# Performance work log

Hardware: AMD Instinct MI355X
Metric: run time of the kernel (lower is better)

The kernel has to match this reference:

```python
import jax, jax.numpy as jnp
import numpy as np
import math

V, T, E, H, L = 32000, 1024, 1024, 16, 6
B = 2
D = E // H
F = 4 * E


def setup_inputs() -> dict:
    key = jax.random.key(0)
    ks = jax.random.split(key, 12)
    s = 0.02
    rn = lambda k, shape: jax.random.normal(k, shape, jnp.float32) * s
    return dict(
        idx=jax.random.randint(ks[0], (B, T), 0, V),
        tok_w=rn(ks[1], (V, E)),
        pos_w=rn(ks[2], (T, E)),
        ln1_g=jnp.ones((L, E)), ln1_b=jnp.zeros((L, E)),
        wq=rn(ks[3], (L, E, E)), wk=rn(ks[4], (L, E, E)), wv=rn(ks[5], (L, E, E)),
        wp=rn(ks[6], (L, E, E)), bp=jnp.zeros((L, E)),
        ln2_g=jnp.ones((L, E)), ln2_b=jnp.zeros((L, E)),
        w1=rn(ks[7], (L, E, F)), b1=jnp.zeros((L, F)),
        w2=rn(ks[8], (L, F, E)), b2=jnp.zeros((L, E)),
        lnf_g=jnp.ones((E,)), lnf_b=jnp.zeros((E,)),
        wlm=rn(ks[9], (E, V)), blm=jnp.zeros((V,)),
    )


def _layernorm(x, g, b, eps=1e-5):
    m = jnp.mean(x, axis=-1, keepdims=True)
    v = jnp.var(x, axis=-1, keepdims=True)
    return (x - m) * jax.lax.rsqrt(v + eps) * g + b


def _forward(idx, tok_w, pos_w, ln1_g, ln1_b, wq, wk, wv, wp, bp,
             ln2_g, ln2_b, w1, b1, w2, b2, lnf_g, lnf_b, wlm, blm):
    Bx, Tx = idx.shape
    x = tok_w[idx] + pos_w[jnp.arange(Tx)][None, :, :]  # [B,T,E]
    causal = jnp.tril(jnp.ones((Tx, Tx), dtype=bool))
    scale = 1.0 / math.sqrt(D)
    for l in range(L):
        h = _layernorm(x, ln1_g[l], ln1_b[l])
        q = (h @ wq[l]).reshape(Bx, Tx, H, D).transpose(0, 2, 1, 3)  # [B,H,T,D]
        k = (h @ wk[l]).reshape(Bx, Tx, H, D).transpose(0, 2, 1, 3)
        v = (h @ wv[l]).reshape(Bx, Tx, H, D).transpose(0, 2, 1, 3)
        att = jnp.einsum('bhtd,bhsd->bhts', q, k) * scale  # [B,H,T,T]
        att = jnp.where(causal, att, -jnp.inf)
        att = jax.nn.softmax(att, axis=-1)
        y = jnp.einsum('bhts,bhsd->bhtd', att, v)
        y = y.transpose(0, 2, 1, 3).reshape(Bx, Tx, E)
        x = x + y @ wp[l] + bp[l]
        h2 = _layernorm(x, ln2_g[l], ln2_b[l])
        ff = jax.nn.gelu(h2 @ w1[l] + b1[l], approximate=False) @ w2[l] + b2[l]
        x = x + ff
    x = _layernorm(x, lnf_g, lnf_b)
    return x @ wlm + blm  # logits [B,T,V]


def reference(idx, tok_w, pos_w, ln1_g, ln1_b, wq, wk, wv, wp, bp,
              ln2_g, ln2_b, w1, b1, w2, b2, lnf_g, lnf_b, wlm, blm):
    return _forward(idx, tok_w, pos_w, ln1_g, ln1_b, wq, wk, wv, wp, bp,
                    ln2_g, ln2_b, w1, b1, w2, b2, lnf_g, lnf_b, wlm, blm)
```

## Files before the change

kernel.cpp:

```cpp
#include <hip/hip_runtime.h>

#define T_SEQ   1024
#define E_DIM   1024
#define H_HEADS 16
#define D_HEAD  64
#define L_LAYERS 6
#define B_BATCH 2
#define F_DIM   4096
#define V_VOCAB 32000

typedef float f32x4 __attribute__((ext_vector_type(4)));
typedef short short8 __attribute__((ext_vector_type(8)));

__device__ __forceinline__ unsigned short f2bf(float f) {
  union { float f; unsigned int u; } v; v.f = f;
  unsigned int r = v.u + 0x7fffu + ((v.u >> 16) & 1u);
  return (unsigned short)(r >> 16);
}

#define GLDS16(gp, lp) __builtin_amdgcn_global_load_lds( \
    (const __attribute__((address_space(1))) void*)(gp), \
    (__attribute__((address_space(3))) void*)(lp), 16, 0, 0)

__global__ void embed_kernel(const int* __restrict__ idx, const float* __restrict__ tok,
                             const float* __restrict__ pos, float* __restrict__ x) {
  int i = blockIdx.x * 256 + threadIdx.x;
  int bt = i >> 8;
  int e4 = i & 255;
  int t  = bt & (T_SEQ - 1);
  int tokid = idx[bt];
  f32x4 a = *(const f32x4*)(tok + (size_t)tokid * E_DIM + e4 * 4);
  f32x4 p = *(const f32x4*)(pos + (size_t)t * E_DIM + e4 * 4);
  *(f32x4*)(x + (size_t)bt * E_DIM + e4 * 4) = a + p;
}

__global__ void ln_kernel(const float* __restrict__ x, const float* __restrict__ g,
                          const float* __restrict__ b, unsigned short* __restrict__ out) {
  int row = blockIdx.x;
  int tid = threadIdx.x;
  const float* xr = x + (size_t)row * E_DIM;
  f32x4 v = *(const f32x4*)(xr + tid * 4);
  float s  = v[0] + v[1] + v[2] + v[3];
  float s2 = v[0]*v[0] + v[1]*v[1] + v[2]*v[2] + v[3]*v[3];
  #pragma unroll
  for (int off = 32; off > 0; off >>= 1) {
    s  += __shfl_xor(s,  off);
    s2 += __shfl_xor(s2, off);
  }
  __shared__ float red[2][4];
  int wave = tid >> 6;
  if ((tid & 63) == 0) { red[0][wave] = s; red[1][wave] = s2; }
  __syncthreads();
  s  = red[0][0] + red[0][1] + red[0][2] + red[0][3];
  s2 = red[1][0] + red[1][1] + red[1][2] + red[1][3];
  float mean = s * (1.0f / E_DIM);
  float var  = s2 * (1.0f / E_DIM) - mean * mean;
  float rstd = rsqrtf(var + 1e-5f);
  f32x4 gv = *(const f32x4*)(g + tid * 4);
  f32x4 bv = *(const f32x4*)(b + tid * 4);
  ushort4 o;
  o.x = f2bf((v[0] - mean) * rstd * gv[0] + bv[0]);
  o.y = f2bf((v[1] - mean) * rstd * gv[1] + bv[1]);
  o.z = f2bf((v[2] - mean) * rstd * gv[2] + bv[2]);
  o.w = f2bf((v[3] - mean) * rstd * gv[3] + bv[3]);
  *(ushort4*)(out + (size_t)row * E_DIM + tid * 4) = o;
}

__device__ __forceinline__ void wtrans_body(const float* __restrict__ W,
    unsigned short* __restrict__ Wt, int K, int N, int bx, int by) {
  __shared__ float tile[64][65];
  const int n0 = bx * 64, k0 = by * 64;
  const int tr  = threadIdx.x >> 4;
  const int tc4 = (threadIdx.x & 15) * 4;
  #pragma unroll
  for (int p = 0; p < 4; ++p) {
    f32x4 v = *(const f32x4*)(W + (size_t)(k0 + p * 16 + tr) * N + n0 + tc4);
    tile[p * 16 + tr][tc4 + 0] = v[0];
    tile[p * 16 + tr][tc4 + 1] = v[1];
    tile[p * 16 + tr][tc4 + 2] = v[2];
    tile[p * 16 + tr][tc4 + 3] = v[3];
  }
  __syncthreads();
  #pragma unroll
  for (int p = 0; p < 4; ++p) {
    int n = p * 16 + tr;
    ushort4 o;
    o.x = f2bf(tile[tc4 + 0][n]);
    o.y = f2bf(tile[tc4 + 1][n]);
    o.z = f2bf(tile[tc4 + 2][n]);
    o.w = f2bf(tile[tc4 + 3][n]);
    *(ushort4*)(Wt + (size_t)(n0 + n) * K + k0 + tc4) = o;
  }
}

__global__ __launch_bounds__(256) void wtrans_kernel(const float* __restrict__ W,
    unsigned short* __restrict__ Wt, int K, int N) {
  wtrans_body(W, Wt, K, N, blockIdx.x, blockIdx.y);
}

__global__ __launch_bounds__(256) void wtrans4_kernel(const float* __restrict__ W0,
    const float* __restrict__ W1, const float* __restrict__ W2, const float* __restrict__ W3,
    unsigned short* __restrict__ Wt) {
  const float* W = blockIdx.z == 0 ? W0 : (blockIdx.z == 1 ? W1 : (blockIdx.z == 2 ? W2 : W3));
  wtrans_body(W, Wt + (size_t)blockIdx.z * E_DIM * E_DIM, E_DIM, E_DIM,
              blockIdx.x, blockIdx.y);
}

__global__ __launch_bounds__(256) void wtrans2_kernel(const float* __restrict__ W1,
    const float* __restrict__ W2, unsigned short* __restrict__ Wt1,
    unsigned short* __restrict__ Wt2) {
  const int id = blockIdx.x;
  if (blockIdx.y == 0) wtrans_body(W1, Wt1, E_DIM, F_DIM, id % (F_DIM / 64), id / (F_DIM / 64));
  else                 wtrans_body(W2, Wt2, F_DIM, E_DIM, id % (E_DIM / 64), id / (E_DIM / 64));
}

__global__ __launch_bounds__(256) void attn_mfma_kernel(
    const unsigned short* __restrict__ qkv, unsigned short* __restrict__ y) {
  __shared__ __align__(16) unsigned short Kl[64 * 64];
  __shared__ __align__(16) unsigned short Vt[64 * 64];
  __shared__ __align__(16) unsigned short pbuf[4][16][72];
  const int tid  = threadIdx.x;
  const int lane = tid & 63;
  const int wave = tid >> 6;
  const int h  = blockIdx.y & (H_HEADS - 1);
  const int b  = blockIdx.y >> 4;
  const int r0 = blockIdx.x * 64 + wave * 16;
  const size_t RS = 3 * E_DIM;
  const unsigned short* q = qkv + (size_t)b * T_SEQ * RS + (size_t)h * D_HEAD;
  const unsigned short* k = q + E_DIM;
  const unsigned short* v = q + 2 * E_DIM;
  const size_t ybase = (size_t)b * T_SEQ * E_DIM + (size_t)h * D_HEAD;
  const int fr = lane & 15, fg = lane >> 4;
  const int rsw = (fr & 7) << 4;

  const int krow = lane >> 3;
  const int kcol = ((lane & 7) * 16) ^ ((krow & 7) << 4);

  short8 aq[2];
  #pragma unroll
  for (int c = 0; c < 2; ++c)
    aq[c] = *(const short8*)(q + (size_t)(r0 + fr) * RS + c * 32 + fg * 8);

  f32x4 oacc[4];
  #pragma unroll
  for (int cg = 0; cg < 4; ++cg) oacc[cg] = (f32x4){0.f, 0.f, 0.f, 0.f};
  float m_ = -1e30f, l_ = 0.0f;

  char* pb = (char*)pbuf + wave * 16 * 144;
  const int ntiles = blockIdx.x + 1;
  for (int t = 0; t < ntiles; ++t) {
    const int j0 = t * 64;
    __syncthreads();
    #pragma unroll
    for (int i = 0; i < 2; ++i) {
      const int row = wave * 16 + i * 8;
      GLDS16((const char*)k + (size_t)(j0 + row + krow) * RS * 2 + kcol,
             (char*)Kl + row * 128);
    }
    {
      short8 v0 = *(const short8*)(v + (size_t)(j0 + lane) * RS + wave * 16);
      short8 v1 = *(const short8*)(v + (size_t)(j0 + lane) * RS + wave * 16 + 8);
      #pragma unroll
      for (int i = 0; i < 8; ++i) {
        const int d0 = wave * 16 + i;
        *(unsigned short*)((char*)Vt + ((d0 * 128 + lane * 2) ^ ((d0 & 7) << 4))) =
            (unsigned short)v0[i];
        const int d1 = wave * 16 + 8 + i;
        *(unsigned short*)((char*)Vt + ((d1 * 128 + lane * 2) ^ ((d1 & 7) << 4))) =
            (unsigned short)v1[i];
      }
    }
    __syncthreads();
    f32x4 st[4];
    #pragma unroll
    for (int c = 0; c < 4; ++c) {
      const char* kb = (char*)Kl + (c * 16 + fr) * 128;
      short8 ka0 = *(const short8*)(kb + ((fg * 16) ^ rsw));
      short8 ka1 = *(const short8*)(kb + ((64 + fg * 16) ^ rsw));
      f32x4 z = (f32x4){0.f, 0.f, 0.f, 0.f};
      z = __builtin_amdgcn_mfma_f32_16x16x32_bf16(ka0, aq[0], z, 0, 0, 0);
      z = __builtin_amdgcn_mfma_f32_16x16x32_bf16(ka1, aq[1], z, 0, 0, 0);
      st[c] = z;
    }
    const int qg = r0 + fr;
    float pv[4][4];
    float mx = -1e30f;
    #pragma unroll
    for (int c = 0; c < 4; ++c)
      #pragma unroll
      for (int r = 0; r < 4; ++r) {
        const int kj = j0 + c * 16 + fg * 4 + r;
        float val = (kj <= qg) ? st[c][r] * 0.125f : -1e30f;
        pv[c][r] = val;
        mx = fmaxf(mx, val);
      }
    mx = fmaxf(mx, __shfl_xor(mx, 16));
    mx = fmaxf(mx, __shfl_xor(mx, 32));
    const float mn = fmaxf(m_, mx);
    const float cfs = __expf(m_ - mn);
    float ls = 0.0f;
    #pragma unroll
    for (int c = 0; c < 4; ++c) {
      ushort4 o;
      float e0 = __expf(pv[c][0] - mn), e1 = __expf(pv[c][1] - mn);
      float e2 = __expf(pv[c][2] - mn), e3 = __expf(pv[c][3] - mn);
      ls += (e0 + e1) + (e2 + e3);
      o.x = f2bf(e0); o.y = f2bf(e1); o.z = f2bf(e2); o.w = f2bf(e3);
      *(ushort4*)(pb + fr * 144 + c * 32 + fg * 8) = o;
    }
    ls += __shfl_xor(ls, 16);
    ls += __shfl_xor(ls, 32);
    l_ = l_ * cfs + ls;
    m_ = mn;
    float cfO[4];
    #pragma unroll
    for (int r = 0; r < 4; ++r) cfO[r] = __shfl(cfs, (lane & 48) | (fg * 4 + r));
    asm volatile("s_waitcnt lgkmcnt(0)" ::: "memory");
    __builtin_amdgcn_sched_barrier(0);
    short8 pa0 = *(const short8*)(pb + fr * 144 + fg * 16);
    short8 pa1 = *(const short8*)(pb + fr * 144 + 64 + fg * 16);
    __builtin_amdgcn_s_setprio(1);
    #pragma unroll
    for (int cg = 0; cg < 4; ++cg) {
      const char* vb = (char*)Vt + (cg * 16 + fr) * 128;
      short8 b0 = *(const short8*)(vb + ((fg * 16) ^ rsw));
      short8 b1 = *(const short8*)(vb + ((64 + fg * 16) ^ rsw));
      #pragma unroll
      for (int r = 0; r < 4; ++r) oacc[cg][r] *= cfO[r];
      oacc[cg] = __builtin_amdgcn_mfma_f32_16x16x32_bf16(pa0, b0, oacc[cg], 0, 0, 0);
      oacc[cg] = __builtin_amdgcn_mfma_f32_16x16x32_bf16(pa1, b1, oacc[cg], 0, 0, 0);
    }
    __builtin_amdgcn_s_setprio(0);
  }
  float lO[4];
  #pragma unroll
  for (int r = 0; r < 4; ++r) lO[r] = __shfl(l_, (lane & 48) | (fg * 4 + r));
  #pragma unroll
  for (int cg = 0; cg < 4; ++cg)
    #pragma unroll
    for (int r = 0; r < 4; ++r)
      y[ybase + (size_t)(r0 + fg * 4 + r) * E_DIM + cg * 16 + fr] = f2bf(oacc[cg][r] / lO[r]);
}

template<int BM, int BN, bool HAS_BIAS, bool GELU_ACT, bool HAS_RES, bool OUT_BF16>
__global__ __launch_bounds__(256) void gemm_bt_kernel(
    const unsigned short* __restrict__ A, const unsigned short* __restrict__ Bt,
    const float* __restrict__ bias, const float* __restrict__ res,
    void* __restrict__ out, int M, int N, int K) {
  constexpr int BK = 64;
  constexpr int MR = BM / 32;
  constexpr int NR = BN / 32;
  constexpr int AI = BM / 32;
  constexpr int BI = BN / 32;
  __shared__ __align__(16) unsigned short As[BM * BK];
  __shared__ __align__(16) unsigned short Bs[BN * BK];
  const int tid  = threadIdx.x;
  const int lane = tid & 63;
  const int wave = tid >> 6;
  const int wr = wave >> 1, wc = wave & 1;

  const int mt = M / BM;
  const int q8 = gridDim.x >> 3;
  const int g  = (blockIdx.x & 7) * q8 + (blockIdx.x >> 3);
  const int m0 = (g % mt) * BM, n0 = (g / mt) * BN;

  const int fr = lane & 15, fg = lane >> 4;
  const int lrow = lane >> 3;
  const int scol = ((lane & 7) * 16) ^ (lrow << 4);
  const size_t K2 = (size_t)K * 2;
  const char* aG = (const char*)A  + (size_t)(m0 + wave * 8 + lrow) * K2 + scol;
  const char* bG = (const char*)Bt + (size_t)(n0 + wave * 8 + lrow) * K2 + scol;

  f32x4 acc[MR][NR];
  #pragma unroll
  for (int mi = 0; mi < MR; ++mi)
    #pragma unroll
    for (int ni = 0; ni < NR; ++ni) acc[mi][ni] = (f32x4){0.f, 0.f, 0.f, 0.f};

  for (int k0 = 0; k0 < K; k0 += BK) {
    __syncthreads();
    #pragma unroll
    for (int i = 0; i < AI; ++i)
      GLDS16(aG + (size_t)i * 32 * K2 + (size_t)k0 * 2, (char*)As + wave * 1024 + i * 4096);
    #pragma unroll
    for (int i = 0; i < BI; ++i)
      GLDS16(bG + (size_t)i * 32 * K2 + (size_t)k0 * 2, (char*)Bs + wave * 1024 + i * 4096);
    __syncthreads();

    short8 af[MR][2], bf[NR][2];
    #pragma unroll
    for (int mi = 0; mi < MR; ++mi) {
      const int row = wr * (BM / 2) + mi * 16 + fr;
      #pragma unroll
      for (int kh = 0; kh < 2; ++kh)
        af[mi][kh] = *(const short8*)((const char*)As + row * 128 +
                       ((kh * 64 + fg * 16) ^ ((row & 7) << 4)));
    }
    #pragma unroll
    for (int ni = 0; ni < NR; ++ni) {
      const int row = wc * (BN / 2) + ni * 16 + fr;
      #pragma unroll
      for (int kh = 0; kh < 2; ++kh)
        bf[ni][kh] = *(const short8*)((const char*)Bs + row * 128 +
                       ((kh * 64 + fg * 16) ^ ((row & 7) << 4)));
    }
    #pragma unroll
    for (int mi = 0; mi < MR; ++mi)
      #pragma unroll
      for (int ni = 0; ni < NR; ++ni) {
        acc[mi][ni] = __builtin_amdgcn_mfma_f32_16x16x32_bf16(af[mi][0], bf[ni][0], acc[mi][ni], 0, 0, 0);
        acc[mi][ni] = __builtin_amdgcn_mfma_f32_16x16x32_bf16(af[mi][1], bf[ni][1], acc[mi][ni], 0, 0, 0);
      }
  }

  #pragma unroll
  for (int mi = 0; mi < MR; ++mi) {
    #pragma unroll
    for (int ni = 0; ni < NR; ++ni) {
      const int col = n0 + wc * (BN / 2) + ni * 16 + fr;
      float bv = HAS_BIAS ? bias[col] : 0.0f;
      #pragma unroll
      for (int r = 0; r < 4; ++r) {
        const int row = m0 + wr * (BM / 2) + mi * 16 + fg * 4 + r;
        float val = acc[mi][ni][r] + bv;
        if (GELU_ACT) val = 0.5f * val * (1.0f + erff(val * 0.70710678118f));
        if (HAS_RES)  val += res[(size_t)row * N + col];
        if (OUT_BF16) ((unsigned short*)out)[(size_t)row * N + col] = f2bf(val);
        else          ((float*)out)[(size_t)row * N + col] = val;
      }
    }
  }
}

__global__ __launch_bounds__(512, 1) void gemm8p_kernel(
    const unsigned short* __restrict__ A, const unsigned short* __restrict__ Bt,
    const float* __restrict__ bias, float* __restrict__ out, int M, int N, int K) {
  __shared__ __align__(16) char lds[131072];
  const int tid  = threadIdx.x;
  const int lane = tid & 63;
  const int wv   = tid >> 6;
  const int wm = wv >> 2, wn = wv & 3;

  const int mt = M >> 8;
  const int q8 = gridDim.x >> 3;
  const int g  = (blockIdx.x & 7) * q8 + (blockIdx.x >> 3);
  const int m0 = (g % mt) * 256, n0 = (g / mt) * 256;

  const int fr = lane & 15, fg = lane >> 4;
  const size_t K2 = (size_t)K * 2;
  const int nIter = K >> 7;

  const int csw0 = (fg * 16) ^ ((fr & 7) << 4);
  const int csw1 = (64 + fg * 16) ^ ((fr & 7) << 4);

  const int sc = (lane * 16) & 127;
  const size_t laneoff = (size_t)(lane >> 3) * K2 + (size_t)(sc ^ ((lane >> 3) << 4));
  const char* Asrc = (const char*)(A + (size_t)m0 * K) + (size_t)(wv * 8) * K2 + laneoff;
  const char* Bsrc = (const char*)(Bt + (size_t)n0 * K) + laneoff;

  f32x4 acc[8][4];
  #pragma unroll
  for (int i = 0; i < 8; ++i)
    #pragma unroll
    for (int j = 0; j < 4; ++j) acc[i][j] = (f32x4){0.f, 0.f, 0.f, 0.f};

  auto stageA = [&](int b, int q, int kt) {
    GLDS16(Asrc + (size_t)(q * 64) * K2 + (size_t)kt * 128,
           lds + b * 65536 + q * 8192 + wv * 1024);
  };
  auto stageB = [&](int b, int j, int o, int kt) {
    const int gw = j * 64 + wv * 8;
    const int rw = ((gw >> 5) << 6) + (gw & 31) + o * 32;
    GLDS16(Bsrc + (size_t)rw * K2 + (size_t)kt * 128,
           lds + b * 65536 + 32768 + rw * 128);
  };

  stageA(0, 0, 0); stageA(0, 2, 0);
  stageB(0, 0, 0, 0); stageB(0, 1, 0, 0);
  stageA(0, 1, 0); stageA(0, 3, 0);
  stageB(0, 0, 1, 0); stageB(0, 1, 1, 0);
  stageA(1, 0, 1); stageA(1, 2, 1);
  stageB(1, 0, 0, 1); stageB(1, 1, 0, 1);
  __builtin_amdgcn_sched_barrier(0);
  asm volatile("s_waitcnt vmcnt(4)" ::: "memory");
  __builtin_amdgcn_s_barrier();

  for (int i = 0; i < nIter; ++i) {
    const bool last = (i == nIter - 1);
    short8 fa[4][2];
    #pragma unroll
    for (int p = 0; p < 8; ++p) {
      const int b  = p >> 2;
      const int mh = (p & 3) >> 1;
      const int nh = p & 1;
      const char* Ab = lds + b * 65536;
      const char* Bb = Ab + 32768;
      __builtin_amdgcn_sched_barrier(0);
      if (nh == 0) {
        #pragma unroll
        for (int j = 0; j < 4; ++j) {
          const int row = wm * 128 + mh * 64 + j * 16 + fr;
          fa[j][0] = *(const short8*)(Ab + row * 128 + csw0);
          fa[j][1] = *(const short8*)(Ab + row * 128 + csw1);
        }
      }
      short8 fb[2][2];
      #pragma unroll
      for (int n = 0; n < 2; ++n) {
        const int row = wn * 64 + nh * 32 + n * 16 + fr;
        fb[n][0] = *(const short8*)(Bb + row * 128 + csw0);
        fb[n][1] = *(const short8*)(Bb + row * 128 + csw1);
      }
      if (p == 0) { stageA(1, 1, 2 * i + 1); stageA(1, 3, 2 * i + 1); }
      if (p == 1) { stageB(1, 0, 1, 2 * i + 1); stageB(1, 1, 1, 2 * i + 1); }
      if (!last) {
        if (p == 2) { stageA(0, 0, 2 * i + 2); stageA(0, 2, 2 * i + 2); }
        if (p == 3) { stageB(0, 0, 0, 2 * i + 2); stageB(0, 1, 0, 2 * i + 2); }
        if (p == 4) { stageA(0, 1, 2 * i + 2); stageA(0, 3, 2 * i + 2); }
        if (p == 5) { stageB(0, 0, 1, 2 * i + 2); stageB(0, 1, 1, 2 * i + 2); }
        if (p == 6) { stageA(1, 0, 2 * i + 3); stageA(1, 2, 2 * i + 3); }
        if (p == 7) { stageB(1, 0, 0, 2 * i + 3); stageB(1, 1, 0, 2 * i + 3); }
      }
      __builtin_amdgcn_sched_barrier(0);
      __builtin_amdgcn_s_barrier();
      __builtin_amdgcn_sched_barrier(0);
      __builtin_amdgcn_s_setprio(1);
      #pragma unroll
      for (int j = 0; j < 4; ++j)
        #pragma unroll
        for (int n = 0; n < 2; ++n) {
          acc[mh * 4 + j][nh * 2 + n] = __builtin_amdgcn_mfma_f32_16x16x32_bf16(
              fa[j][0], fb[n][0], acc[mh * 4 + j][nh * 2 + n], 0, 0, 0);
          acc[mh * 4 + j][nh * 2 + n] = __builtin_amdgcn_mfma_f32_16x16x32_bf16(
              fa[j][1], fb[n][1], acc[mh * 4 + j][nh * 2 + n], 0, 0, 0);
        }
      __builtin_amdgcn_s_setprio(0);
      __builtin_amdgcn_sched_barrier(0);
      if (p == 3) {
        if (!last) asm volatile("s_waitcnt vmcnt(4)" ::: "memory");
        else       asm volatile("s_waitcnt vmcnt(0)" ::: "memory");
      }
      if (p == 7 && !last)
        asm volatile("s_waitcnt vmcnt(4)" ::: "memory");
      __builtin_amdgcn_s_barrier();
    }
  }

  #pragma unroll
  for (int mi = 0; mi < 8; ++mi) {
    #pragma unroll
    for (int ni = 0; ni < 4; ++ni) {
      const int col = n0 + wn * 64 + ni * 16 + fr;
      const float bv = bias[col];
      #pragma unroll
      for (int r = 0; r < 4; ++r) {
        const int row = m0 + wm * 128 + mi * 16 + fg * 4 + r;
        out[(size_t)row * N + col] = acc[mi][ni][r] + bv;
      }
    }
  }
}

extern "C" void kernel_launch(void* const* d_in, const int* in_sizes, int n_in,
                              void* d_out, int out_size, void* d_ws, size_t ws_size,
                              hipStream_t stream) {
  const int*   idx   = (const int*)  d_in[0];
  const float* tok_w = (const float*)d_in[1];
  const float* pos_w = (const float*)d_in[2];
  const float* ln1_g = (const float*)d_in[3];
  const float* ln1_b = (const float*)d_in[4];
  const float* wq    = (const float*)d_in[5];
  const float* wk    = (const float*)d_in[6];
  const float* wv    = (const float*)d_in[7];
  const float* wp    = (const float*)d_in[8];
  const float* bp    = (const float*)d_in[9];
  const float* ln2_g = (const float*)d_in[10];
  const float* ln2_b = (const float*)d_in[11];
  const float* w1    = (const float*)d_in[12];
  const float* b1    = (const float*)d_in[13];
  const float* w2    = (const float*)d_in[14];
  const float* b2    = (const float*)d_in[15];
  const float* lnf_g = (const float*)d_in[16];
  const float* lnf_b = (const float*)d_in[17];
  const float* wlm   = (const float*)d_in[18];
  const float* blm   = (const float*)d_in[19];

  const int M = B_BATCH * T_SEQ;
  const size_t EE = (size_t)E_DIM * E_DIM;
  const size_t EF = (size_t)E_DIM * F_DIM;
  char* p = (char*)d_ws;
  float* x            = (float*)p;          p += (size_t)M * E_DIM * 4;
  unsigned short* hb  = (unsigned short*)p; p += (size_t)M * E_DIM * 2;
  unsigned short* qkv = (unsigned short*)p; p += (size_t)M * 3 * E_DIM * 2;
  unsigned short* yb  = (unsigned short*)p; p += (size_t)M * E_DIM * 2;
  unsigned short* tb  = (unsigned short*)p; p += (size_t)M * F_DIM * 2;
  unsigned short* wtb = (unsigned short*)p; p += (size_t)V_VOCAB * E_DIM * 2;

  embed_kernel<<<M * E_DIM / 4 / 256, 256, 0, stream>>>(idx, tok_w, pos_w, x);

  dim3 g_a(T_SEQ / 64, B_BATCH * H_HEADS);
  for (int l = 0; l < L_LAYERS; ++l) {
    ln_kernel<<<M, 256, 0, stream>>>(x, ln1_g + (size_t)l * E_DIM, ln1_b + (size_t)l * E_DIM, hb);
    wtrans4_kernel<<<dim3(E_DIM / 64, E_DIM / 64, 4), 256, 0, stream>>>(
        wq + l * EE, wk + l * EE, wv + l * EE, wp + l * EE, wtb);
    gemm_bt_kernel<128, 128, false, false, false, true>
        <<<(M / 128) * (3 * E_DIM / 128), 256, 0, stream>>>(
        hb, wtb, nullptr, nullptr, qkv, M, 3 * E_DIM, E_DIM);
    attn_mfma_kernel<<<g_a, 256, 0, stream>>>(qkv, yb);
    gemm_bt_kernel<64, 128, true, false, true, false>
        <<<(M / 64) * (E_DIM / 128), 256, 0, stream>>>(
        yb, wtb + 3 * EE, bp + (size_t)l * E_DIM, x, x, M, E_DIM, E_DIM);
    ln_kernel<<<M, 256, 0, stream>>>(x, ln2_g + (size_t)l * E_DIM, ln2_b + (size_t)l * E_DIM, hb);
    wtrans2_kernel<<<dim3(1024, 2), 256, 0, stream>>>(
        w1 + l * EF, w2 + l * EF, wtb, wtb + EF);
    gemm_bt_kernel<128, 128, true, true, false, true>
        <<<(M / 128) * (F_DIM / 128), 256, 0, stream>>>(
        hb, wtb, b1 + (size_t)l * F_DIM, nullptr, tb, M, F_DIM, E_DIM);
    gemm_bt_kernel<64, 128, true, false, true, false>
        <<<(M / 64) * (E_DIM / 128), 256, 0, stream>>>(
        tb, wtb + EF, b2 + (size_t)l * E_DIM, x, x, M, E_DIM, F_DIM);
  }
  ln_kernel<<<M, 256, 0, stream>>>(x, lnf_g, lnf_b, hb);
  wtrans_kernel<<<dim3(V_VOCAB / 64, E_DIM / 64), 256, 0, stream>>>(wlm, wtb, E_DIM, V_VOCAB);
  gemm8p_kernel<<<(M / 256) * (V_VOCAB / 256), 512, 0, stream>>>(
      hb, wtb, blm, (float*)d_out, M, V_VOCAB, E_DIM);
}
```

Baseline: 1.404 ms.

## Write V transposed from QKV GEMM and pair causal query tiles per attention block

The QKV GEMM epilogue now writes Q and K into a 2E-stride buffer and V directly in a per-head transposed [D,T] layout. The attention kernel can then load V tiles into LDS with async global-to-LDS copies instead of doing scalar transposes. Attention blocks now hold 8 waves, pairing query tile bx with tile 15-bx so every block does the same causal work, and the grid is halved. The lm-head GEMM also reloads A fragments on every phase instead of caching them across phases, which trades register pressure against LDS traffic. Risks are uncoalesced strided V stores in the GEMM epilogue and idle waves in the paired blocks on early tiles.

```diff
diff --git a/kernel.cpp b/kernel.cpp
--- a/kernel.cpp
+++ b/kernel.cpp
@@ -114,27 +114,31 @@
   else                 wtrans_body(W2, Wt2, F_DIM, E_DIM, id % (E_DIM / 64), id / (E_DIM / 64));
 }
 
-__global__ __launch_bounds__(256) void attn_mfma_kernel(
-    const unsigned short* __restrict__ qkv, unsigned short* __restrict__ y) {
+__global__ __launch_bounds__(512) void attn_mfma_kernel(
+    const unsigned short* __restrict__ qk, const unsigned short* __restrict__ vt,
+    unsigned short* __restrict__ y) {
   __shared__ __align__(16) unsigned short Kl[64 * 64];
-  __shared__ __align__(16) unsigned short Vt[64 * 64];
-  __shared__ __align__(16) unsigned short pbuf[4][16][72];
+  __shared__ __align__(16) unsigned short Vl[64 * 64];
+  __shared__ __align__(16) unsigned short pbuf[8][16][72];
   const int tid  = threadIdx.x;
   const int lane = tid & 63;
   const int wave = tid >> 6;
+  const int grp  = wave >> 2;
+  const int wl   = wave & 3;
+  const int bx = blockIdx.x;
   const int h  = blockIdx.y & (H_HEADS - 1);
   const int b  = blockIdx.y >> 4;
-  const int r0 = blockIdx.x * 64 + wave * 16;
-  const size_t RS = 3 * E_DIM;
-  const unsigned short* q = qkv + (size_t)b * T_SEQ * RS + (size_t)h * D_HEAD;
+  const int qt = grp == 0 ? (15 - bx) : bx;
+  const int r0 = qt * 64 + wl * 16;
+  const size_t RS = 2 * E_DIM;
+  const unsigned short* q = qk + (size_t)b * T_SEQ * RS + (size_t)h * D_HEAD;
   const unsigned short* k = q + E_DIM;
-  const unsigned short* v = q + 2 * E_DIM;
+  const unsigned short* vb = vt + (size_t)(b * H_HEADS + h) * D_HEAD * T_SEQ;
   const size_t ybase = (size_t)b * T_SEQ * E_DIM + (size_t)h * D_HEAD;
   const int fr = lane & 15, fg = lane >> 4;
   const int rsw = (fr & 7) << 4;
-
-  const int krow = lane >> 3;
-  const int kcol = ((lane & 7) * 16) ^ ((krow & 7) << 4);
+  const int srow = lane >> 3;
+  const int ssw  = ((lane & 7) * 16) ^ (srow << 4);
 
   short8 aq[2];
   #pragma unroll
@@ -147,90 +151,77 @@
   float m_ = -1e30f, l_ = 0.0f;
 
   char* pb = (char*)pbuf + wave * 16 * 144;
-  const int ntiles = blockIdx.x + 1;
+  const int ntiles = 16 - bx;
   for (int t = 0; t < ntiles; ++t) {
     const int j0 = t * 64;
     __syncthreads();
-    #pragma unroll
-    for (int i = 0; i < 2; ++i) {
-      const int row = wave * 16 + i * 8;
-      GLDS16((const char*)k + (size_t)(j0 + row + krow) * RS * 2 + kcol,
-             (char*)Kl + row * 128);
+    GLDS16((const char*)k + (size_t)(j0 + wave * 8 + srow) * RS * 2 + ssw,
+           (char*)Kl + wave * 8 * 128);
+    GLDS16((const char*)vb + ((size_t)(wave * 8 + srow) * T_SEQ + j0) * 2 + ssw,
+           (char*)Vl + wave * 8 * 128);
+    __syncthreads();
+    if (t <= qt) {
+      f32x4 st[4];
+      #pragma unroll
+      for (int c = 0; c < 4; ++c) {
+        const char* kb = (char*)Kl + (c * 16 + fr) * 128;
+        short8 ka0 = *(const short8*)(kb + ((fg * 16) ^ rsw));
+        short8 ka1 = *(const short8*)(kb + ((64 + fg * 16) ^ rsw));
+        f32x4 z = (f32x4){0.f, 0.f, 0.f, 0.f};
+        z = __builtin_amdgcn_mfma_f32_16x16x32_bf16(ka0, aq[0], z, 0, 0, 0);
+        z = __builtin_amdgcn_mfma_f32_16x16x32_bf16(ka1, aq[1], z, 0, 0, 0);
+        st[c] = z;
+      }
+      const int qg = r0 + fr;
+      float pv[4][4];
+      float mx = -1e30f;
+      #pragma unroll
+      for (int c = 0; c < 4; ++c)
+        #pragma unroll
+        for (int r = 0; r < 4; ++r) {
+          const int kj = j0 + c * 16 + fg * 4 + r;
+          float val = (kj <= qg) ? st[c][r] * 0.125f : -1e30f;
+          pv[c][r] = val;
+          mx = fmaxf(mx, val);
+        }
+      mx = fmaxf(mx, __shfl_xor(mx, 16));
+      mx = fmaxf(mx, __shfl_xor(mx, 32));
+      const float mn = fmaxf(m_, mx);
+      const float cfs = __expf(m_ - mn);
+      float ls = 0.0f;
+      #pragma unroll
+      for (int c = 0; c < 4; ++c) {
+        ushort4 o;
+        float e0 = __expf(pv[c][0] - mn), e1 = __expf(pv[c][1] - mn);
+        float e2 = __expf(pv[c][2] - mn), e3 = __expf(pv[c][3] - mn);
+        ls += (e0 + e1) + (e2 + e3);
+        o.x = f2bf(e0); o.y = f2bf(e1); o.z = f2bf(e2); o.w = f2bf(e3);
+        *(ushort4*)(pb + fr * 144 + c * 32 + fg * 8) = o;
+      }
+      ls += __shfl_xor(ls, 16);
+      ls += __shfl_xor(ls, 32);
+      l_ = l_ * cfs + ls;
+      m_ = mn;
+      float cfO[4];
+      #pragma unroll
+      for (int r = 0; r < 4; ++r) cfO[r] = __shfl(cfs, (lane & 48) | (fg * 4 + r));
+      asm volatile("s_waitcnt lgkmcnt(0)" ::: "memory");
+      __builtin_amdgcn_sched_barrier(0);
+      short8 pa0 = *(const short8*)(pb + fr * 144 + fg * 16);
+      short8 pa1 = *(const short8*)(pb + fr * 144 + 64 + fg * 16);
+      __builtin_amdgcn_s_setprio(1);
+      #pragma unroll
+      for (int cg = 0; cg < 4; ++cg) {
+        const char* vv = (char*)Vl + (cg * 16 + fr) * 128;
+        short8 b0 = *(const short8*)(vv + ((fg * 16) ^ rsw));
+        short8 b1 = *(const short8*)(vv + ((64 + fg * 16) ^ rsw));
+        #pragma unroll
+        for (int r = 0; r < 4; ++r) oacc[cg][r] *= cfO[r];
+        oacc[cg] = __builtin_amdgcn_mfma_f32_16x16x32_bf16(pa0, b0, oacc[cg], 0, 0, 0);
+        oacc[cg] = __builtin_amdgcn_mfma_f32_16x16x32_bf16(pa1, b1, oacc[cg], 0, 0, 0);
+      }
+      __builtin_amdgcn_s_setprio(0);
     }
-    {
-      short8 v0 = *(const short8*)(v + (size_t)(j0 + lane) * RS + wave * 16);
-      short8 v1 = *(const short8*)(v + (size_t)(j0 + lane) * RS + wave * 16 + 8);
-      #pragma unroll
-      for (int i = 0; i < 8; ++i) {
-        const int d0 = wave * 16 + i;
-        *(unsigned short*)((char*)Vt + ((d0 * 128 + lane * 2) ^ ((d0 & 7) << 4))) =
-            (unsigned short)v0[i];
-        const int d1 = wave * 16 + 8 + i;
-        *(unsigned short*)((char*)Vt + ((d1 * 128 + lane * 2) ^ ((d1 & 7) << 4))) =
-            (unsigned short)v1[i];
-      }
-    }
-    __syncthreads();
-    f32x4 st[4];
-    #pragma unroll
-    for (int c = 0; c < 4; ++c) {
-      const char* kb = (char*)Kl + (c * 16 + fr) * 128;
-      short8 ka0 = *(const short8*)(kb + ((fg * 16) ^ rsw));
-      short8 ka1 = *(const short8*)(kb + ((64 + fg * 16) ^ rsw));
-      f32x4 z = (f32x4){0.f, 0.f, 0.f, 0.f};
-      z = __builtin_amdgcn_mfma_f32_16x16x32_bf16(ka0, aq[0], z, 0, 0, 0);
-      z = __builtin_amdgcn_mfma_f32_16x16x32_bf16(ka1, aq[1], z, 0, 0, 0);
-      st[c] = z;
-    }
-    const int qg = r0 + fr;
-    float pv[4][4];
-    float mx = -1e30f;
-    #pragma unroll
-    for (int c = 0; c < 4; ++c)
-      #pragma unroll
-      for (int r = 0; r < 4; ++r) {
-        const int kj = j0 + c * 16 + fg * 4 + r;
-        float val = (kj <= qg) ? st[c][r] * 0.125f : -1e30f;
-        pv[c][r] = val;
-        mx = fmaxf(mx, val);
-      }
-    mx = fmaxf(mx, __shfl_xor(mx, 16));
-    mx = fmaxf(mx, __shfl_xor(mx, 32));
-    const float mn = fmaxf(m_, mx);
-    const float cfs = __expf(m_ - mn);
-    float ls = 0.0f;
-    #pragma unroll
-    for (int c = 0; c < 4; ++c) {
-      ushort4 o;
-      float e0 = __expf(pv[c][0] - mn), e1 = __expf(pv[c][1] - mn);
-      float e2 = __expf(pv[c][2] - mn), e3 = __expf(pv[c][3] - mn);
-      ls += (e0 + e1) + (e2 + e3);
-      o.x = f2bf(e0); o.y = f2bf(e1); o.z = f2bf(e2); o.w = f2bf(e3);
-      *(ushort4*)(pb + fr * 144 + c * 32 + fg * 8) = o;
-    }
-    ls += __shfl_xor(ls, 16);
-    ls += __shfl_xor(ls, 32);
-    l_ = l_ * cfs + ls;
-    m_ = mn;
-    float cfO[4];
-    #pragma unroll
-    for (int r = 0; r < 4; ++r) cfO[r] = __shfl(cfs, (lane & 48) | (fg * 4 + r));
-    asm volatile("s_waitcnt lgkmcnt(0)" ::: "memory");
-    __builtin_amdgcn_sched_barrier(0);
-    short8 pa0 = *(const short8*)(pb + fr * 144 + fg * 16);
-    short8 pa1 = *(const short8*)(pb + fr * 144 + 64 + fg * 16);
-    __builtin_amdgcn_s_setprio(1);
-    #pragma unroll
-    for (int cg = 0; cg < 4; ++cg) {
-      const char* vb = (char*)Vt + (cg * 16 + fr) * 128;
-      short8 b0 = *(const short8*)(vb + ((fg * 16) ^ rsw));
-      short8 b1 = *(const short8*)(vb + ((64 + fg * 16) ^ rsw));
-      #pragma unroll
-      for (int r = 0; r < 4; ++r) oacc[cg][r] *= cfO[r];
-      oacc[cg] = __builtin_amdgcn_mfma_f32_16x16x32_bf16(pa0, b0, oacc[cg], 0, 0, 0);
-      oacc[cg] = __builtin_amdgcn_mfma_f32_16x16x32_bf16(pa1, b1, oacc[cg], 0, 0, 0);
-    }
-    __builtin_amdgcn_s_setprio(0);
   }
   float lO[4];
   #pragma unroll
@@ -242,11 +233,11 @@
       y[ybase + (size_t)(r0 + fg * 4 + r) * E_DIM + cg * 16 + fr] = f2bf(oacc[cg][r] / lO[r]);
 }
 
-template<int BM, int BN, bool HAS_BIAS, bool GELU_ACT, bool HAS_RES, bool OUT_BF16>
+template<int BM, int BN, bool HAS_BIAS, bool GELU_ACT, bool HAS_RES, int OMODE>
 __global__ __launch_bounds__(256) void gemm_bt_kernel(
     const unsigned short* __restrict__ A, const unsigned short* __restrict__ Bt,
     const float* __restrict__ bias, const float* __restrict__ res,
-    void* __restrict__ out, int M, int N, int K) {
+    void* __restrict__ out, unsigned short* __restrict__ vt, int M, int N, int K) {
   constexpr int BK = 64;
   constexpr int MR = BM / 32;
   constexpr int NR = BN / 32;
@@ -319,14 +310,37 @@
     for (int ni = 0; ni < NR; ++ni) {
       const int col = n0 + wc * (BN / 2) + ni * 16 + fr;
       float bv = HAS_BIAS ? bias[col] : 0.0f;
+      float vals[4];
+      const int rbase = m0 + wr * (BM / 2) + mi * 16 + fg * 4;
       #pragma unroll
       for (int r = 0; r < 4; ++r) {
-        const int row = m0 + wr * (BM / 2) + mi * 16 + fg * 4 + r;
         float val = acc[mi][ni][r] + bv;
         if (GELU_ACT) val = 0.5f * val * (1.0f + erff(val * 0.70710678118f));
-        if (HAS_RES)  val += res[(size_t)row * N + col];
-        if (OUT_BF16) ((unsigned short*)out)[(size_t)row * N + col] = f2bf(val);
-        else          ((float*)out)[(size_t)row * N + col] = val;
+        if (HAS_RES)  val += res[(size_t)(rbase + r) * N + col];
+        vals[r] = val;
+      }
+      if (OMODE == 0) {
+        #pragma unroll
+        for (int r = 0; r < 4; ++r)
+          ((float*)out)[(size_t)(rbase + r) * N + col] = vals[r];
+      } else if (OMODE == 1) {
+        #pragma unroll
+        for (int r = 0; r < 4; ++r)
+          ((unsigned short*)out)[(size_t)(rbase + r) * N + col] = f2bf(vals[r]);
+      } else {
+        if (col < 2 * E_DIM) {
+          #pragma unroll
+          for (int r = 0; r < 4; ++r)
+            ((unsigned short*)out)[(size_t)(rbase + r) * 2 * E_DIM + col] = f2bf(vals[r]);
+        } else {
+          const int c2 = col - 2 * E_DIM;
+          const int hh = c2 >> 6, d = c2 & 63;
+          const int bb = rbase >> 10, t0 = rbase & (T_SEQ - 1);
+          ushort4 o;
+          o.x = f2bf(vals[0]); o.y = f2bf(vals[1]);
+          o.z = f2bf(vals[2]); o.w = f2bf(vals[3]);
+          *(ushort4*)(vt + ((size_t)(bb * H_HEADS + hh) * D_HEAD + d) * T_SEQ + t0) = o;
+        }
       }
     }
   }
@@ -387,7 +401,6 @@
 
   for (int i = 0; i < nIter; ++i) {
     const bool last = (i == nIter - 1);
-    short8 fa[4][2];
     #pragma unroll
     for (int p = 0; p < 8; ++p) {
       const int b  = p >> 2;
@@ -396,15 +409,13 @@
       const char* Ab = lds + b * 65536;
       const char* Bb = Ab + 32768;
       __builtin_amdgcn_sched_barrier(0);
-      if (nh == 0) {
-        #pragma unroll
-        for (int j = 0; j < 4; ++j) {
-          const int row = wm * 128 + mh * 64 + j * 16 + fr;
-          fa[j][0] = *(const short8*)(Ab + row * 128 + csw0);
-          fa[j][1] = *(const short8*)(Ab + row * 128 + csw1);
-        }
-      }
-      short8 fb[2][2];
+      short8 fa[4][2], fb[2][2];
+      #pragma unroll
+      for (int j = 0; j < 4; ++j) {
+        const int row = wm * 128 + mh * 64 + j * 16 + fr;
+        fa[j][0] = *(const short8*)(Ab + row * 128 + csw0);
+        fa[j][1] = *(const short8*)(Ab + row * 128 + csw1);
+      }
       #pragma unroll
       for (int n = 0; n < 2; ++n) {
         const int row = wn * 64 + nh * 32 + n * 16 + fr;
@@ -491,34 +502,34 @@
   char* p = (char*)d_ws;
   float* x            = (float*)p;          p += (size_t)M * E_DIM * 4;
   unsigned short* hb  = (unsigned short*)p; p += (size_t)M * E_DIM * 2;
-  unsigned short* qkv = (unsigned short*)p; p += (size_t)M * 3 * E_DIM * 2;
+  unsigned short* qkb = (unsigned short*)p; p += (size_t)M * 2 * E_DIM * 2;
+  unsigned short* vtb = (unsigned short*)p; p += (size_t)M * E_DIM * 2;
   unsigned short* yb  = (unsigned short*)p; p += (size_t)M * E_DIM * 2;
   unsigned short* tb  = (unsigned short*)p; p += (size_t)M * F_DIM * 2;
   unsigned short* wtb = (unsigned short*)p; p += (size_t)V_VOCAB * E_DIM * 2;
 
   embed_kernel<<<M * E_DIM / 4 / 256, 256, 0, stream>>>(idx, tok_w, pos_w, x);
 
-  dim3 g_a(T_SEQ / 64, B_BATCH * H_HEADS);
   for (int l = 0; l < L_LAYERS; ++l) {
     ln_kernel<<<M, 256, 0, stream>>>(x, ln1_g + (size_t)l * E_DIM, ln1_b + (size_t)l * E_DIM, hb);
     wtrans4_kernel<<<dim3(E_DIM / 64, E_DIM / 64, 4), 256, 0, stream>>>(
         wq + l * EE, wk + l * EE, wv + l * EE, wp + l * EE, wtb);
-    gemm_bt_kernel<128, 128, false, false, false, true>
+    gemm_bt_kernel<128, 128, false, false, false, 2>
         <<<(M / 128) * (3 * E_DIM / 128), 256, 0, stream>>>(
-        hb, wtb, nullptr, nullptr, qkv, M, 3 * E_DIM, E_DIM);
-    attn_mfma_kernel<<<g_a, 256, 0, stream>>>(qkv, yb);
-    gemm_bt_kernel<64, 128, true, false, true, false>
+        hb, wtb, nullptr, nullptr, qkb, vtb, M, 3 * E_DIM, E_DIM);
+    attn_mfma_kernel<<<dim3(8, B_BATCH * H_HEADS), 512, 0, stream>>>(qkb, vtb, yb);
+    gemm_bt_kernel<64, 128, true, false, true, 0>
         <<<(M / 64) * (E_DIM / 128), 256, 0, stream>>>(
-        yb, wtb + 3 * EE, bp + (size_t)l * E_DIM, x, x, M, E_DIM, E_DIM);
+        yb, wtb + 3 * EE, bp + (size_t)l * E_DIM, x, x, nullptr, M, E_DIM, E_DIM);
     ln_kernel<<<M, 256, 0, stream>>>(x, ln2_g + (size_t)l * E_DIM, ln2_b + (size_t)l * E_DIM, hb);
     wtrans2_kernel<<<dim3(1024, 2), 256, 0, stream>>>(
         w1 + l * EF, w2 + l * EF, wtb, wtb + EF);
-    gemm_bt_kernel<128, 128, true, true, false, true>
+    gemm_bt_kernel<128, 128, true, true, false, 1>
         <<<(M / 128) * (F_DIM / 128), 256, 0, stream>>>(
-        hb, wtb, b1 + (size_t)l * F_DIM, nullptr, tb, M, F_DIM, E_DIM);
-    gemm_bt_kernel<64, 128, true, false, true, false>
+        hb, wtb, b1 + (size_t)l * F_DIM, nullptr, tb, nullptr, M, F_DIM, E_DIM);
+    gemm_bt_kernel<64, 128, true, false, true, 0>
         <<<(M / 64) * (E_DIM / 128), 256, 0, stream>>>(
-        tb, wtb + EF, b2 + (size_t)l * E_DIM, x, x, M, E_DIM, F_DIM);
+        tb, wtb + EF, b2 + (size_t)l * E_DIM, x, x, nullptr, M, E_DIM, F_DIM);
   }
   ln_kernel<<<M, 256, 0, stream>>>(x, lnf_g, lnf_b, hb);
   wtrans_kernel<<<dim3(V_VOCAB / 64, E_DIM / 64), 256, 0, stream>>>(wlm, wtb, E_DIM, V_VOCAB);
```

After: 1.357 ms. -3.4%, faster.
